# Performance work log

Measured on AMD Instinct MI355X. Metric: run time of the kernel, lower is better.

Reference implementation:

```python
import jax, jax.numpy as jnp
import numpy as np

NUM_GRAPHS = 64
HID = 6
NUM_CLASSES = 10
NUM_FEATS = 128


def setup_inputs() -> dict:
    key = jax.random.key(0)
    ks = jax.random.split(key, 20)
    N, E = 100000, 3200000
    x = jax.random.normal(ks[0], (N, NUM_FEATS), dtype=jnp.float32)
    edge_index = jax.random.randint(ks[1], (2, E), 0, N, dtype=jnp.int64)
    batch = jnp.sort(jax.random.randint(ks[2], (N,), 0, NUM_GRAPHS, dtype=jnp.int64))
    def glorot(k, fan_in, fan_out):
        lim = np.sqrt(6.0 / (fan_in + fan_out))
        return jax.random.uniform(k, (fan_in, fan_out), jnp.float32, -lim, lim)
    inp = {"x": x, "edge_index": edge_index, "batch": batch}
    dims = [(NUM_FEATS, HID)] + [(HID, HID)] * 5 + [(HID, NUM_CLASSES)]
    names = ["1", "2", "3", "4", "5", "6", "f"]
    for i, (nm, (fi, fo)) in enumerate(zip(names, dims)):
        inp["W" + nm] = glorot(ks[3 + i], fi, fo)
        inp["b" + nm] = jnp.zeros((fo,), jnp.float32)
    return inp


def _gcn_forward(x, edge_index, batch, Ws, bs):
    N = x.shape[0]
    loop = jnp.arange(N, dtype=edge_index.dtype)
    src = jnp.concatenate([edge_index[0], loop])  # self-loops appended
    dst = jnp.concatenate([edge_index[1], loop])
    deg = jax.ops.segment_sum(jnp.ones_like(dst, dtype=x.dtype), dst, num_segments=N)
    dinv = jnp.where(deg > 0, jax.lax.rsqrt(deg), 0.0)
    norm = dinv[src] * dinv[dst]  # [E+N]

    def conv(h, W, b):
        h = h @ W  # [N, out]
        agg = jax.ops.segment_sum(h[src] * norm[:, None], dst, num_segments=N)
        return agg + b

    h = x
    for W, b in zip(Ws, bs):
        h = jax.nn.relu(conv(h, W, b))

    # global mean pool over graphs
    sums = jax.ops.segment_sum(h, batch, num_segments=NUM_GRAPHS)
    cnts = jax.ops.segment_sum(jnp.ones((N,), h.dtype), batch, num_segments=NUM_GRAPHS)
    pooled = sums / jnp.maximum(cnts, 1.0)[:, None]
    return jax.nn.log_softmax(pooled, axis=1)


def reference(x, edge_index, batch, W1, b1, W2, b2, W3, b3, W4, b4, W5, b5, W6, b6, Wf, bf):
    Ws = [W1, W2, W3, W4, W5, W6, Wf]
    bs = [b1, b2, b3, b4, b5, b6, bf]
    return _gcn_forward(x, edge_index, batch, Ws, bs)
```

## Files before the change

kernel.cpp:

```cpp
#include <hip/hip_runtime.h>
#include <hip/hip_bf16.h>
#include <hip/hip_fp16.h>
#include <math.h>

#define NF     128
#define HID    6
#define NC     10
#define NG     64
#define SLOTS  64
#define OVFCAP 8192

#define BKT_SH    7
#define BKT_NODES 128
#define NBK_MAX   1024
#define EPB       4096
#define BCAP      5120
#define BOVFCAP   4096

__device__ __forceinline__ void addh2(__half2& a0, __half2& a1, __half2& a2, uint4 q) {
    const __half2* h = (const __half2*)&q;
    a0 = __hadd2(a0, h[0]);
    a1 = __hadd2(a1, h[1]);
    a2 = __hadd2(a2, h[2]);
}

__device__ __forceinline__ __half2 shfl_xor_h2(__half2 v, int m) {
    union { __half2 h; unsigned int u; } a;
    a.h = v;
    a.u = __shfl_xor(a.u, m);
    return a.h;
}

__device__ __forceinline__ uint4 packh(const float* v) {
    uint4 q;
    __half2* h = (__half2*)&q;
    h[0] = __floats2half2_rn(v[0], v[1]);
    h[1] = __floats2half2_rn(v[2], v[3]);
    h[2] = __floats2half2_rn(v[4], v[5]);
    h[3] = __floats2half2_rn(0.f, 0.f);
    return q;
}

__global__ __launch_bounds__(256) void bucket_scatter_kernel(
        const int* __restrict__ src, const int* __restrict__ dst, int E, int nbk,
        int* __restrict__ bucket_cursor, unsigned int* __restrict__ bucket_arr,
        int* __restrict__ bovf_meta, int2* __restrict__ bovf) {
    __shared__ int cntL[NBK_MAX];
    __shared__ int offs[NBK_MAX];
    __shared__ int gb[NBK_MAX];
    __shared__ int wtot[4];
    __shared__ unsigned int stage[EPB];
    __shared__ unsigned int stage_gi[EPB];
    int tid = threadIdx.x;
    for (int k = tid; k < NBK_MAX; k += 256) cntL[k] = 0;
    __syncthreads();
    int e0 = blockIdx.x * EPB;
    int cnt_e = E - e0; if (cnt_e > EPB) cnt_e = EPB;
    int sreg[16], dreg[16], rank[16];
    if (cnt_e == EPB && (E & 3) == 0) {
        const int4* s4p = (const int4*)(src + e0);
        const int4* d4p = (const int4*)(dst + e0);
#pragma unroll
        for (int k = 0; k < 4; ++k) {
            int4 sv = s4p[k * 256 + tid];
            int4 dv = d4p[k * 256 + tid];
            sreg[4*k+0] = sv.x; sreg[4*k+1] = sv.y; sreg[4*k+2] = sv.z; sreg[4*k+3] = sv.w;
            dreg[4*k+0] = dv.x; dreg[4*k+1] = dv.y; dreg[4*k+2] = dv.z; dreg[4*k+3] = dv.w;
        }
#pragma unroll
        for (int k = 0; k < 16; ++k) rank[k] = atomicAdd(&cntL[dreg[k] >> BKT_SH], 1);
    } else {
#pragma unroll
        for (int k = 0; k < 16; ++k) {
            int e = e0 + k * 256 + tid;
            if (e < E) {
                dreg[k] = dst[e]; sreg[k] = src[e];
                rank[k] = atomicAdd(&cntL[dreg[k] >> BKT_SH], 1);
            } else dreg[k] = -1;
        }
    }
    __syncthreads();
    int base = tid * 4;
    int c0 = cntL[base], c1 = cntL[base + 1], c2 = cntL[base + 2], c3 = cntL[base + 3];
    int tsum = c0 + c1 + c2 + c3;
    int lane = tid & 63, wv = tid >> 6;
    int v = tsum;
#pragma unroll
    for (int off = 1; off < 64; off <<= 1) {
        int u = __shfl_up(v, off);
        if (lane >= off) v += u;
    }
    if (lane == 63) wtot[wv] = v;
    __syncthreads();
    int wbase = 0;
    for (int w = 0; w < wv; ++w) wbase += wtot[w];
    int ex = wbase + v - tsum;
    offs[base]     = ex;
    offs[base + 1] = ex + c0;
    offs[base + 2] = ex + c0 + c1;
    offs[base + 3] = ex + c0 + c1 + c2;
    for (int bb = tid; bb < nbk; bb += 256) {
        int c = cntL[bb];
        if (c > 0) gb[bb] = atomicAdd(&bucket_cursor[bb], c);
    }
    __syncthreads();
#pragma unroll
    for (int k = 0; k < 16; ++k) {
        int d = dreg[k];
        if (d < 0) continue;
        int b = d >> BKT_SH;
        int pos = offs[b] + rank[k];
        unsigned int p = (unsigned int)(d & (BKT_NODES - 1)) | ((unsigned int)sreg[k] << BKT_SH);
        int grel = gb[b] + rank[k];
        stage[pos] = p;
        if (grel < BCAP) {
            stage_gi[pos] = (unsigned int)b * BCAP + (unsigned int)grel;
        } else {
            stage_gi[pos] = 0xFFFFFFFFu;
            int p2 = atomicAdd(bovf_meta, 1);
            if (p2 < BOVFCAP) bovf[p2] = make_int2(d, sreg[k]);
        }
    }
    __syncthreads();
    for (int j = tid; j < cnt_e; j += 256) {
        unsigned int gi = stage_gi[j];
        if (gi != 0xFFFFFFFFu) bucket_arr[gi] = stage[j];
    }
}

__global__ __launch_bounds__(256) void ell_build_kernel(
        const unsigned int* __restrict__ bucket_arr, const int* __restrict__ bucket_cursor,
        const int* __restrict__ bovf_meta, const int2* __restrict__ bovf,
        int* __restrict__ ell, int* __restrict__ cnt, float* __restrict__ dinv,
        int* __restrict__ ovf_meta, int* __restrict__ ovf_dst, int* __restrict__ ovf_src,
        int N) {
    __shared__ int ell_s[BKT_NODES * SLOTS];
    __shared__ int cur[BKT_NODES];
    int b = blockIdx.x;
    int tid = threadIdx.x;
    if (tid < BKT_NODES) cur[tid] = 0;
    for (int k = tid; k < BKT_NODES * SLOTS; k += 256) ell_s[k] = N;
    __syncthreads();
    int bc = bucket_cursor[b];
    if (bc > BCAP) bc = BCAP;
    const unsigned int* ba = bucket_arr + (size_t)b * BCAP;
    int bc4 = bc >> 2;
    const uint4* ba4 = (const uint4*)ba;
    for (int j = tid; j < bc4; j += 256) {
        uint4 pv = ba4[j];
        unsigned int ps[4] = { pv.x, pv.y, pv.z, pv.w };
#pragma unroll
        for (int q = 0; q < 4; ++q) {
            unsigned int p = ps[q];
            int r = (int)(p & (BKT_NODES - 1));
            int s = (int)(p >> BKT_SH);
            int slot = atomicAdd(&cur[r], 1);
            if (slot < SLOTS) {
                ell_s[r * SLOTS + slot] = s;
            } else {
                int d = (b << BKT_SH) + r;
                int qq = atomicAdd(ovf_meta, 1);
                if (qq < OVFCAP) { ovf_dst[qq] = d; ovf_src[qq] = s; }
            }
        }
    }
    for (int j = (bc4 << 2) + tid; j < bc; j += 256) {
        unsigned int p = ba[j];
        int r = (int)(p & (BKT_NODES - 1));
        int s = (int)(p >> BKT_SH);
        int slot = atomicAdd(&cur[r], 1);
        if (slot < SLOTS) {
            ell_s[r * SLOTS + slot] = s;
        } else {
            int d = (b << BKT_SH) + r;
            int q = atomicAdd(ovf_meta, 1);
            if (q < OVFCAP) { ovf_dst[q] = d; ovf_src[q] = s; }
        }
    }
    int m = *bovf_meta;
    if (m > BOVFCAP) m = BOVFCAP;
    for (int t = tid; t < m; t += 256) {
        int2 e = bovf[t];
        if ((e.x >> BKT_SH) == b) {
            int r = e.x & (BKT_NODES - 1);
            int slot = atomicAdd(&cur[r], 1);
            if (slot < SLOTS) {
                ell_s[r * SLOTS + slot] = e.y;
            } else {
                int q = atomicAdd(ovf_meta, 1);
                if (q < OVFCAP) { ovf_dst[q] = e.x; ovf_src[q] = e.y; }
            }
        }
    }
    __syncthreads();
    int nid0 = b << BKT_SH;
    int rows = N - nid0; if (rows > BKT_NODES) rows = BKT_NODES;
    if (rows <= 0) return;
    int4* eg = (int4*)(ell + (size_t)nid0 * SLOTS);
    const int4* es = (const int4*)ell_s;
    for (int k = tid; k < rows * (SLOTS / 4); k += 256) {
        int r = k >> 4;
        int q = k & 15;
        int c = cur[r]; if (c > SLOTS) c = SLOTS;
        if (q * 4 < c) eg[k] = es[k];
    }
    for (int r = tid; r < rows; r += 256) {
        int deg = cur[r];
        cnt[nid0 + r] = deg;
        dinv[nid0 + r] = rsqrtf((float)deg + 1.0f);
    }
}

__global__ __launch_bounds__(256) void layer1_kernel(const float* __restrict__ x,
                                                     const float* __restrict__ W,
                                                     const float* __restrict__ dinv,
                                                     uint4* __restrict__ g16, int N) {
    __shared__ float sW[8 * 100];
    for (int idx = threadIdx.x; idx < NF * HID; idx += 256) {
        int s = idx / 96, r = idx % 96;
        int o = r / 16, j = r % 16;
        sW[s * 100 + o * 16 + j] = W[(s * 16 + j) * HID + o];
    }
    __syncthreads();
    int t = blockIdx.x * 256 + threadIdx.x;
    int i = t >> 3;
    int sub = t & 7;
    if (t == 0) g16[N] = make_uint4(0u, 0u, 0u, 0u);
    if (i >= N) return;
    const float4* xr = (const float4*)(x + (size_t)i * NF + sub * 16);
    float4 xv0 = xr[0], xv1 = xr[1], xv2 = xr[2], xv3 = xr[3];
    const float4* wr = (const float4*)(sW + sub * 100);
    float p[HID];
#pragma unroll
    for (int o = 0; o < HID; ++o) {
        float4 w0 = wr[o * 4 + 0], w1 = wr[o * 4 + 1], w2 = wr[o * 4 + 2], w3 = wr[o * 4 + 3];
        p[o] = xv0.x * w0.x + xv0.y * w0.y + xv0.z * w0.z + xv0.w * w0.w
             + xv1.x * w1.x + xv1.y * w1.y + xv1.z * w1.z + xv1.w * w1.w
             + xv2.x * w2.x + xv2.y * w2.y + xv2.z * w2.z + xv2.w * w2.w
             + xv3.x * w3.x + xv3.y * w3.y + xv3.z * w3.z + xv3.w * w3.w;
    }
#pragma unroll
    for (int m = 1; m < 8; m <<= 1) {
#pragma unroll
        for (int o = 0; o < HID; ++o) p[o] += __shfl_xor(p[o], m);
    }
    if (sub == 0) {
        float dv = dinv[i];
        float v[HID];
#pragma unroll
        for (int o = 0; o < HID; ++o) v[o] = dv * p[o];
        g16[i] = packh(v);
    }
}

__device__ __forceinline__ void gather8h(int ne, const int* __restrict__ er,
                                         const uint4* __restrict__ g16, int sub,
                                         __half2& a0, __half2& a1, __half2& a2) {
#pragma unroll
    for (int r = 0; r < SLOTS / 32; ++r) {
        int base = r * 32 + sub * 4;
        if (base < ne) {
            int4 q = *(const int4*)(er + base);
            uint4 v0 = g16[q.x];
            uint4 v1 = g16[q.y];
            uint4 v2 = g16[q.z];
            uint4 v3 = g16[q.w];
            addh2(a0, a1, a2, v0);
            addh2(a0, a1, a2, v1);
            addh2(a0, a1, a2, v2);
            addh2(a0, a1, a2, v3);
        }
    }
}

template<int PREP>
__global__ __launch_bounds__(256) void gcn_layer8_kernel(
        const int* __restrict__ cnt, const int* __restrict__ ell,
        const int* __restrict__ ovf_meta, const int* __restrict__ ovf_dst,
        const int* __restrict__ ovf_src, const float* __restrict__ dinv,
        const uint4* __restrict__ gin, uint4* __restrict__ gout,
        const float* __restrict__ W, const float* __restrict__ b, int N) {
    int t = blockIdx.x * 256 + threadIdx.x;
    int i = t >> 3;
    int sub = t & 7;
    if (t == 0) gout[N] = make_uint4(0u, 0u, 0u, 0u);
    if (i >= N) return;
    int n = cnt[i];
    int ne = n < SLOTS ? n : SLOTS;
    const int* er = ell + (size_t)i * SLOTS;
    __half2 a0 = __float2half2_rn(0.f), a1 = a0, a2 = a0;
    gather8h(ne, er, gin, sub, a0, a1, a2);
    if (sub == 0) addh2(a0, a1, a2, gin[i]);
    if (n > SLOTS && sub == 2) {
        int m = ovf_meta[0];
        m = m < OVFCAP ? m : OVFCAP;
        for (int tt = 0; tt < m; ++tt) {
            if (ovf_dst[tt] == i) addh2(a0, a1, a2, gin[ovf_src[tt]]);
        }
    }
#pragma unroll
    for (int m = 1; m < 8; m <<= 1) {
        a0 = __hadd2(a0, shfl_xor_h2(a0, m));
        a1 = __hadd2(a1, shfl_xor_h2(a1, m));
        a2 = __hadd2(a2, shfl_xor_h2(a2, m));
    }
    if (sub != 0) return;
    float2 f0 = __half22float2(a0), f1 = __half22float2(a1), f2 = __half22float2(a2);
    float acc[HID] = { f0.x, f0.y, f1.x, f1.y, f2.x, f2.y };
    float dv = dinv[i];
    float h[HID];
#pragma unroll
    for (int f = 0; f < HID; ++f) {
        float u = dv * acc[f] + b[f];
        h[f] = u > 0.0f ? u : 0.0f;
    }
    float o[HID];
    if (PREP) {
#pragma unroll
        for (int f = 0; f < HID; ++f) o[f] = dv * h[f];
    } else {
#pragma unroll
        for (int fo = 0; fo < HID; ++fo) {
            float s = 0.0f;
#pragma unroll
            for (int fi = 0; fi < HID; ++fi) s += h[fi] * W[fi * HID + fo];
            o[fo] = dv * s;
        }
    }
    gout[i] = packh(o);
}

__global__ __launch_bounds__(256) void pool_kernel(
        const int* __restrict__ cnt, const int* __restrict__ ell,
        const int* __restrict__ ovf_meta, const int* __restrict__ ovf_dst,
        const int* __restrict__ ovf_src, const float* __restrict__ dinv,
        const uint4* __restrict__ gin, const int* __restrict__ batch,
        const float* __restrict__ Wf, const float* __restrict__ bf,
        float* __restrict__ pooled, float* __restrict__ gcnt, int N) {
    __shared__ float sp[NG * NC];
    __shared__ float sc[NG];
    __shared__ int srange[2];
    for (int k = threadIdx.x; k < NG * NC; k += 256) sp[k] = 0.0f;
    if (threadIdx.x < NG) sc[threadIdx.x] = 0.0f;
    int start = blockIdx.x * 32;
    int endi = min(start + 32, N) - 1;
    if (threadIdx.x == 0) {
        srange[0] = batch[start];
        srange[1] = batch[endi];
    }
    __syncthreads();
    int t = blockIdx.x * 256 + threadIdx.x;
    int i = t >> 3;
    int sub = t & 7;
    if (i < N) {
        int n = cnt[i];
        int ne = n < SLOTS ? n : SLOTS;
        const int* er = ell + (size_t)i * SLOTS;
        __half2 a0 = __float2half2_rn(0.f), a1 = a0, a2 = a0;
        gather8h(ne, er, gin, sub, a0, a1, a2);
        if (sub == 0) addh2(a0, a1, a2, gin[i]);
        if (n > SLOTS && sub == 2) {
            int m = ovf_meta[0];
            m = m < OVFCAP ? m : OVFCAP;
            for (int tt = 0; tt < m; ++tt) {
                if (ovf_dst[tt] == i) addh2(a0, a1, a2, gin[ovf_src[tt]]);
            }
        }
#pragma unroll
        for (int m = 1; m < 8; m <<= 1) {
            a0 = __hadd2(a0, shfl_xor_h2(a0, m));
            a1 = __hadd2(a1, shfl_xor_h2(a1, m));
            a2 = __hadd2(a2, shfl_xor_h2(a2, m));
        }
        if (sub == 0) {
            float2 f0 = __half22float2(a0), f1 = __half22float2(a1), f2 = __half22float2(a2);
            float acc[HID] = { f0.x, f0.y, f1.x, f1.y, f2.x, f2.y };
            float dv = dinv[i];
            float u[HID];
#pragma unroll
            for (int f = 0; f < HID; ++f) u[f] = dv * acc[f];
            int bg = batch[i];
#pragma unroll
            for (int c = 0; c < NC; ++c) {
                float v = bf[c];
#pragma unroll
                for (int f = 0; f < HID; ++f) v += u[f] * Wf[f * NC + c];
                v = v > 0.0f ? v : 0.0f;
                atomicAdd(&sp[bg * NC + c], v);
            }
            atomicAdd(&sc[bg], 1.0f);
        }
    }
    __syncthreads();
    int bmin = srange[0], bmax = srange[1];
    int rows = bmax - bmin + 1;
    for (int k = threadIdx.x; k < rows * NC; k += 256) {
        int r = bmin + k / NC, c = k % NC;
        float v = sp[r * NC + c];
        if (v != 0.0f) atomicAdd(&pooled[r * NC + c], v);
    }
    for (int k = threadIdx.x; k < rows; k += 256) {
        float v = sc[bmin + k];
        if (v != 0.0f) atomicAdd(&gcnt[bmin + k], v);
    }
}

__global__ void logsm_kernel(const float* __restrict__ pooled, const float* __restrict__ gcnt,
                             float* __restrict__ out) {
    int gidx = threadIdx.x;
    if (gidx >= NG) return;
    float c = gcnt[gidx];
    c = c > 1.0f ? c : 1.0f;
    float v[NC];
    float m = -1e30f;
#pragma unroll
    for (int k = 0; k < NC; ++k) {
        v[k] = pooled[gidx * NC + k] / c;
        m = v[k] > m ? v[k] : m;
    }
    float s = 0.0f;
#pragma unroll
    for (int k = 0; k < NC; ++k) s += expf(v[k] - m);
    float ls = logf(s);
#pragma unroll
    for (int k = 0; k < NC; ++k) out[gidx * NC + k] = v[k] - m - ls;
}

extern "C" void kernel_launch(void* const* d_in, const int* in_sizes, int n_in,
                              void* d_out, int out_size, void* d_ws, size_t ws_size,
                              hipStream_t stream) {
    const float* x     = (const float*)d_in[0];
    const int*   ei    = (const int*)d_in[1];
    const int*   batch = (const int*)d_in[2];
    const float* W[7];
    const float* b[7];
    for (int l = 0; l < 7; ++l) {
        W[l] = (const float*)d_in[3 + 2 * l];
        b[l] = (const float*)d_in[4 + 2 * l];
    }
    const int N = in_sizes[2];
    const int E = in_sizes[1] / 2;
    const int nbk = (N + BKT_NODES - 1) >> BKT_SH;
    const int* src = ei;
    const int* dst = ei + E;
    float* out = (float*)d_out;

    char* wp = (char*)d_ws;
    int* bucket_cursor = (int*)wp;  wp += (size_t)NBK_MAX * 4;
    int* ovf_meta  = (int*)wp;      wp += 16;
    int* bovf_meta = (int*)wp;      wp += 16;
    int* ovf_dst   = (int*)wp;      wp += OVFCAP * 4;
    int* ovf_src   = (int*)wp;      wp += OVFCAP * 4;
    int2* bovf     = (int2*)wp;     wp += (size_t)BOVFCAP * 8;
    int* cnt       = (int*)wp;      wp += (((size_t)N * 4 + 15) & ~15ull);
    float* dinv    = (float*)wp;    wp += (((size_t)N * 4 + 15) & ~15ull);
    uint4* g_a     = (uint4*)wp;    wp += (size_t)(N + 1) * 16;
    uint4* g_b     = (uint4*)wp;    wp += (size_t)(N + 1) * 16;
    float* pooled  = (float*)wp;    wp += NG * NC * 4;
    float* gcnt    = (float*)wp;    wp += (((size_t)NG * 4 + 15) & ~15ull);
    int* ell       = (int*)wp;      wp += (size_t)N * SLOTS * 4;
    unsigned int* bucket_arr = (unsigned int*)wp;  wp += (size_t)nbk * BCAP * 4;

    hipMemsetAsync(bucket_cursor, 0, (size_t)NBK_MAX * 4 + 32, stream);
    hipMemsetAsync(pooled, 0, (NG * NC + NG) * sizeof(float), stream);

    const int BT = 256;
    int bn8 = ((size_t)N * 8 + BT - 1) / BT;
    int bp1 = (E + EPB - 1) / EPB;

    bucket_scatter_kernel<<<bp1, BT, 0, stream>>>(src, dst, E, nbk, bucket_cursor,
                                                  bucket_arr, bovf_meta, bovf);
    ell_build_kernel<<<nbk, BT, 0, stream>>>(bucket_arr, bucket_cursor, bovf_meta, bovf,
                                             ell, cnt, dinv, ovf_meta, ovf_dst, ovf_src, N);

    layer1_kernel<<<bn8, BT, 0, stream>>>(x, W[0], dinv, g_a, N);

    gcn_layer8_kernel<0><<<bn8, BT, 0, stream>>>(cnt, ell, ovf_meta, ovf_dst, ovf_src, dinv, g_a, g_b, W[1], b[0], N);
    gcn_layer8_kernel<0><<<bn8, BT, 0, stream>>>(cnt, ell, ovf_meta, ovf_dst, ovf_src, dinv, g_b, g_a, W[2], b[1], N);
    gcn_layer8_kernel<0><<<bn8, BT, 0, stream>>>(cnt, ell, ovf_meta, ovf_dst, ovf_src, dinv, g_a, g_b, W[3], b[2], N);
    gcn_layer8_kernel<0><<<bn8, BT, 0, stream>>>(cnt, ell, ovf_meta, ovf_dst, ovf_src, dinv, g_b, g_a, W[4], b[3], N);
    gcn_layer8_kernel<0><<<bn8, BT, 0, stream>>>(cnt, ell, ovf_meta, ovf_dst, ovf_src, dinv, g_a, g_b, W[5], b[4], N);
    gcn_layer8_kernel<1><<<bn8, BT, 0, stream>>>(cnt, ell, ovf_meta, ovf_dst, ovf_src, dinv, g_b, g_a, nullptr, b[5], N);
    pool_kernel<<<bn8, BT, 0, stream>>>(cnt, ell, ovf_meta, ovf_dst, ovf_src, dinv, g_a, batch, W[6], b[6], pooled, gcnt, N);
    logsm_kernel<<<1, 64, 0, stream>>>(pooled, gcnt, out);
}
```

Measured before the change: 327.9 us.

## Recompute dinv from degree counts and replace memsets with an init kernel

Removes the stored dinv array and instead computes rsqrt(cnt+1) inline in each layer kernel from the degree count already loaded there, saving one N-sized global read per layer. The two hipMemsetAsync calls are replaced by one small init kernel to cut launch overhead. The shared-memory ELL initialisation is also vectorised to int4 stores. In exchange, each layer does a few extra rsqrt instructions.

```diff
diff --git a/kernel.cpp b/kernel.cpp
--- a/kernel.cpp
+++ b/kernel.cpp
@@ -16,6 +16,7 @@
 #define EPB       4096
 #define BCAP      5120
 #define BOVFCAP   4096
+
 
 __device__ __forceinline__ void addh2(__half2& a0, __half2& a1, __half2& a2, uint4 q) {
     const __half2* h = (const __half2*)&q;
@@ -39,6 +40,14 @@
     h[2] = __floats2half2_rn(v[4], v[5]);
     h[3] = __floats2half2_rn(0.f, 0.f);
     return q;
+}
+
+__global__ __launch_bounds__(256) void init_kernel(int* __restrict__ bucket_cursor,
+                                                   float* __restrict__ pooled) {
+    int t = blockIdx.x * 256 + threadIdx.x;
+    if (t < NBK_MAX + 8) bucket_cursor[t] = 0;
+    int p = t - (NBK_MAX + 8);
+    if (p >= 0 && p < NG * NC + NG) pooled[p] = 0.0f;
 }
 
 __global__ __launch_bounds__(256) void bucket_scatter_kernel(
@@ -131,7 +140,7 @@
 __global__ __launch_bounds__(256) void ell_build_kernel(
         const unsigned int* __restrict__ bucket_arr, const int* __restrict__ bucket_cursor,
         const int* __restrict__ bovf_meta, const int2* __restrict__ bovf,
-        int* __restrict__ ell, int* __restrict__ cnt, float* __restrict__ dinv,
+        int* __restrict__ ell, int* __restrict__ cnt,
         int* __restrict__ ovf_meta, int* __restrict__ ovf_dst, int* __restrict__ ovf_src,
         int N) {
     __shared__ int ell_s[BKT_NODES * SLOTS];
@@ -139,7 +148,11 @@
     int b = blockIdx.x;
     int tid = threadIdx.x;
     if (tid < BKT_NODES) cur[tid] = 0;
-    for (int k = tid; k < BKT_NODES * SLOTS; k += 256) ell_s[k] = N;
+    {
+        int4* e4 = (int4*)ell_s;
+        int4 sv = make_int4(N, N, N, N);
+        for (int k = tid; k < BKT_NODES * SLOTS / 4; k += 256) e4[k] = sv;
+    }
     __syncthreads();
     int bc = bucket_cursor[b];
     if (bc > BCAP) bc = BCAP;
@@ -205,15 +218,13 @@
         if (q * 4 < c) eg[k] = es[k];
     }
     for (int r = tid; r < rows; r += 256) {
-        int deg = cur[r];
-        cnt[nid0 + r] = deg;
-        dinv[nid0 + r] = rsqrtf((float)deg + 1.0f);
+        cnt[nid0 + r] = cur[r];
     }
 }
 
 __global__ __launch_bounds__(256) void layer1_kernel(const float* __restrict__ x,
                                                      const float* __restrict__ W,
-                                                     const float* __restrict__ dinv,
+                                                     const int* __restrict__ cnt,
                                                      uint4* __restrict__ g16, int N) {
     __shared__ float sW[8 * 100];
     for (int idx = threadIdx.x; idx < NF * HID; idx += 256) {
@@ -245,7 +256,7 @@
         for (int o = 0; o < HID; ++o) p[o] += __shfl_xor(p[o], m);
     }
     if (sub == 0) {
-        float dv = dinv[i];
+        float dv = rsqrtf((float)cnt[i] + 1.0f);
         float v[HID];
 #pragma unroll
         for (int o = 0; o < HID; ++o) v[o] = dv * p[o];
@@ -277,7 +288,7 @@
 __global__ __launch_bounds__(256) void gcn_layer8_kernel(
         const int* __restrict__ cnt, const int* __restrict__ ell,
         const int* __restrict__ ovf_meta, const int* __restrict__ ovf_dst,
-        const int* __restrict__ ovf_src, const float* __restrict__ dinv,
+        const int* __restrict__ ovf_src,
         const uint4* __restrict__ gin, uint4* __restrict__ gout,
         const float* __restrict__ W, const float* __restrict__ b, int N) {
     int t = blockIdx.x * 256 + threadIdx.x;
@@ -307,7 +318,7 @@
     if (sub != 0) return;
     float2 f0 = __half22float2(a0), f1 = __half22float2(a1), f2 = __half22float2(a2);
     float acc[HID] = { f0.x, f0.y, f1.x, f1.y, f2.x, f2.y };
-    float dv = dinv[i];
+    float dv = rsqrtf((float)n + 1.0f);
     float h[HID];
 #pragma unroll
     for (int f = 0; f < HID; ++f) {
@@ -333,7 +344,7 @@
 __global__ __launch_bounds__(256) void pool_kernel(
         const int* __restrict__ cnt, const int* __restrict__ ell,
         const int* __restrict__ ovf_meta, const int* __restrict__ ovf_dst,
-        const int* __restrict__ ovf_src, const float* __restrict__ dinv,
+        const int* __restrict__ ovf_src,
         const uint4* __restrict__ gin, const int* __restrict__ batch,
         const float* __restrict__ Wf, const float* __restrict__ bf,
         float* __restrict__ pooled, float* __restrict__ gcnt, int N) {
@@ -375,7 +386,7 @@
         if (sub == 0) {
             float2 f0 = __half22float2(a0), f1 = __half22float2(a1), f2 = __half22float2(a2);
             float acc[HID] = { f0.x, f0.y, f1.x, f1.y, f2.x, f2.y };
-            float dv = dinv[i];
+            float dv = rsqrtf((float)n + 1.0f);
             float u[HID];
 #pragma unroll
             for (int f = 0; f < HID; ++f) u[f] = dv * acc[f];
@@ -453,7 +464,6 @@
     int* ovf_src   = (int*)wp;      wp += OVFCAP * 4;
     int2* bovf     = (int2*)wp;     wp += (size_t)BOVFCAP * 8;
     int* cnt       = (int*)wp;      wp += (((size_t)N * 4 + 15) & ~15ull);
-    float* dinv    = (float*)wp;    wp += (((size_t)N * 4 + 15) & ~15ull);
     uint4* g_a     = (uint4*)wp;    wp += (size_t)(N + 1) * 16;
     uint4* g_b     = (uint4*)wp;    wp += (size_t)(N + 1) * 16;
     float* pooled  = (float*)wp;    wp += NG * NC * 4;
@@ -461,26 +471,25 @@
     int* ell       = (int*)wp;      wp += (size_t)N * SLOTS * 4;
     unsigned int* bucket_arr = (unsigned int*)wp;  wp += (size_t)nbk * BCAP * 4;
 
-    hipMemsetAsync(bucket_cursor, 0, (size_t)NBK_MAX * 4 + 32, stream);
-    hipMemsetAsync(pooled, 0, (NG * NC + NG) * sizeof(float), stream);
-
     const int BT = 256;
     int bn8 = ((size_t)N * 8 + BT - 1) / BT;
     int bp1 = (E + EPB - 1) / EPB;
 
+    init_kernel<<<(NBK_MAX + 8 + NG * NC + NG + BT - 1) / BT, BT, 0, stream>>>(bucket_cursor, pooled);
+
     bucket_scatter_kernel<<<bp1, BT, 0, stream>>>(src, dst, E, nbk, bucket_cursor,
                                                   bucket_arr, bovf_meta, bovf);
     ell_build_kernel<<<nbk, BT, 0, stream>>>(bucket_arr, bucket_cursor, bovf_meta, bovf,
-                                             ell, cnt, dinv, ovf_meta, ovf_dst, ovf_src, N);
-
-    layer1_kernel<<<bn8, BT, 0, stream>>>(x, W[0], dinv, g_a, N);
-
-    gcn_layer8_kernel<0><<<bn8, BT, 0, stream>>>(cnt, ell, ovf_meta, ovf_dst, ovf_src, dinv, g_a, g_b, W[1], b[0], N);
-    gcn_layer8_kernel<0><<<bn8, BT, 0, stream>>>(cnt, ell, ovf_meta, ovf_dst, ovf_src, dinv, g_b, g_a, W[2], b[1], N);
-    gcn_layer8_kernel<0><<<bn8, BT, 0, stream>>>(cnt, ell, ovf_meta, ovf_dst, ovf_src, dinv, g_a, g_b, W[3], b[2], N);
-    gcn_layer8_kernel<0><<<bn8, BT, 0, stream>>>(cnt, ell, ovf_meta, ovf_dst, ovf_src, dinv, g_b, g_a, W[4], b[3], N);
-    gcn_layer8_kernel<0><<<bn8, BT, 0, stream>>>(cnt, ell, ovf_meta, ovf_dst, ovf_src, dinv, g_a, g_b, W[5], b[4], N);
-    gcn_layer8_kernel<1><<<bn8, BT, 0, stream>>>(cnt, ell, ovf_meta, ovf_dst, ovf_src, dinv, g_b, g_a, nullptr, b[5], N);
-    pool_kernel<<<bn8, BT, 0, stream>>>(cnt, ell, ovf_meta, ovf_dst, ovf_src, dinv, g_a, batch, W[6], b[6], pooled, gcnt, N);
+                                             ell, cnt, ovf_meta, ovf_dst, ovf_src, N);
+
+    layer1_kernel<<<bn8, BT, 0, stream>>>(x, W[0], cnt, g_a, N);
+
+    gcn_layer8_kernel<0><<<bn8, BT, 0, stream>>>(cnt, ell, ovf_meta, ovf_dst, ovf_src, g_a, g_b, W[1], b[0], N);
+    gcn_layer8_kernel<0><<<bn8, BT, 0, stream>>>(cnt, ell, ovf_meta, ovf_dst, ovf_src, g_b, g_a, W[2], b[1], N);
+    gcn_layer8_kernel<0><<<bn8, BT, 0, stream>>>(cnt, ell, ovf_meta, ovf_dst, ovf_src, g_a, g_b, W[3], b[2], N);
+    gcn_layer8_kernel<0><<<bn8, BT, 0, stream>>>(cnt, ell, ovf_meta, ovf_dst, ovf_src, g_b, g_a, W[4], b[3], N);
+    gcn_layer8_kernel<0><<<bn8, BT, 0, stream>>>(cnt, ell, ovf_meta, ovf_dst, ovf_src, g_a, g_b, W[5], b[4], N);
+    gcn_layer8_kernel<1><<<bn8, BT, 0, stream>>>(cnt, ell, ovf_meta, ovf_dst, ovf_src, g_b, g_a, nullptr, b[5], N);
+    pool_kernel<<<bn8, BT, 0, stream>>>(cnt, ell, ovf_meta, ovf_dst, ovf_src, g_a, batch, W[6], b[6], pooled, gcnt, N);
     logsm_kernel<<<1, 64, 0, stream>>>(pooled, gcnt, out);
 }
```

After: 321.0 us. 2.1% less time.
